# Optimization experiments

Hardware: AMD Instinct MI355X
Metric: run time of the kernel (lower is better)

Reference implementation:

```python
import jax, jax.numpy as jnp
import numpy as np

N_NODES = 100000
N_EDGES = 1600000
IN_FEATS = 128
HEADS = 4
OUT_FEATS = 32
NEG_SLOPE = 0.2


def setup_inputs() -> dict:
    key = jax.random.key(0)
    k1, k2, k3, k4, k5, k6 = jax.random.split(key, 6)
    feat = jax.random.normal(k1, (N_NODES, IN_FEATS), dtype=jnp.float32)
    # nn.Linear(in_feats, out_feats*num_heads).weight -> [H*D_out, D_in]
    W = jax.random.normal(k2, (HEADS * OUT_FEATS, IN_FEATS), dtype=jnp.float32) * (1.0 / np.sqrt(IN_FEATS))
    attn_l = jax.random.normal(k3, (1, HEADS, OUT_FEATS), dtype=jnp.float32) * 0.1
    attn_r = jax.random.normal(k4, (1, HEADS, OUT_FEATS), dtype=jnp.float32) * 0.1
    src = jax.random.randint(k5, (N_EDGES,), 0, N_NODES, dtype=jnp.int32)
    dst = jax.random.randint(k6, (N_EDGES,), 0, N_NODES, dtype=jnp.int32)
    return {"feat": feat, "W": W, "attn_l": attn_l, "attn_r": attn_r, "src": src, "dst": dst}


def reference(feat, W, attn_l, attn_r, src, dst):
    N = feat.shape[0]
    H, D = attn_l.shape[1], attn_l.shape[2]
    # fc: feat @ W.T -> [N, H, D]
    ft = (feat @ W.T).reshape(N, H, D)
    el = jnp.sum(ft * attn_l, axis=-1)  # [N, H]
    er = jnp.sum(ft * attn_r, axis=-1)  # [N, H]
    # SDDMM edge scores (u_add_v) + leaky relu
    e = el[src] + er[dst]  # [E, H]
    e = jnp.where(e > 0, e, NEG_SLOPE * e)
    # segment softmax over edges grouped by destination node
    emax = jax.ops.segment_max(e, dst, num_segments=N)  # [N, H]
    ez = jnp.exp(e - emax[dst])
    esum = jax.ops.segment_sum(ez, dst, num_segments=N)  # [N, H]
    a = ez / esum[dst]  # [E, H]
    # weighted SpMM aggregation (u_mul_e + sum by dst)
    out = jax.ops.segment_sum(ft[src] * a[:, :, None], dst, num_segments=N)  # [N, H, D]
    return out
```

## Files before the change

kernel.cpp:

```cpp
#include <hip/hip_runtime.h>
#include <hip/hip_fp16.h>

#define IN_FEATS 128
#define HEADS 4
#define D_OUT 32
#define HD 128
#define NEG_SLOPE 0.2f

#define BSHIFT 6
#define BSIZE 64
#define CAP 1280
#define NBMAX 1600

#define BSCAT 6
#define MAXCHUNK 3200

typedef _Float16 half8 __attribute__((ext_vector_type(8)));
typedef _Float16 half4v __attribute__((ext_vector_type(4)));
typedef float floatx4 __attribute__((ext_vector_type(4)));

#define LSTR 40
#define OSTR 136
#define SMEM_BYTES (128 * OSTR * 2)

__global__ void init_cursor(int* __restrict__ bcursor, int NB) {
    int b = blockIdx.x * blockDim.x + threadIdx.x;
    if (b < NB) bcursor[b] = b * CAP;
}

__global__ __launch_bounds__(256) void mega(const float* __restrict__ feat,
                                            const float* __restrict__ W,
                                            const float* __restrict__ al,
                                            const float* __restrict__ ar,
                                            const int* __restrict__ src,
                                            const int* __restrict__ dst,
                                            __half* __restrict__ ft_h,
                                            float* __restrict__ el,
                                            float* __restrict__ er,
                                            int* __restrict__ bcursor,
                                            int* __restrict__ bedge,
                                            int N, int E, int NB,
                                            int gemmBlocks, int chunk) {
    __shared__ __align__(16) char smem[SMEM_BYTES];
    const int t = threadIdx.x;

    if (blockIdx.x >= gemmBlocks) {
        int* cnt = (int*)smem;
        int* base = cnt + NBMAX;
        int bid = blockIdx.x - gemmBlocks;
        int e0 = bid * chunk;
        if (e0 >= E) return;
        int e1 = e0 + chunk; if (e1 > E) e1 = E;
        int ne = e1 - e0;
        for (int b = t; b < NB; b += 256) cnt[b] = 0;
        __syncthreads();
        for (int i = t; i < ne; i += 256)
            atomicAdd(&cnt[dst[e0 + i] >> BSHIFT], 1);
        __syncthreads();
        for (int b = t; b < NB; b += 256) {
            int c = cnt[b];
            base[b] = c ? atomicAdd(&bcursor[b], c) : 0;
        }
        __syncthreads();
        for (int b = t; b < NB; b += 256) cnt[b] = 0;
        __syncthreads();
        for (int i = t; i < ne; i += 256) {
            int d = dst[e0 + i];
            int b = d >> BSHIFT;
            int p = base[b] + atomicAdd(&cnt[b], 1);
            if (p < (b + 1) * CAP)
                bedge[p] = src[e0 + i] | ((d & (BSIZE - 1)) << 17);
        }
        return;
    }

    _Float16* sh = (_Float16*)smem;
    _Float16* Als = sh;
    _Float16* Wls = sh + 5120;
    const int w = t >> 6, lane = t & 63, quad = lane >> 4, l15 = lane & 15;
    const int nodeBase = blockIdx.x * 128;

    floatx4 acc[2][8] = {};

    for (int kk = 0; kk < 4; ++kk) {
        const int k0 = kk * 32;
#pragma unroll
        for (int i = 0; i < 4; ++i) {
            int idx = i * 256 + t;
            int row = idx >> 3;
            int q = idx & 7;
            int node = nodeBase + row;
            float4 v = make_float4(0.f, 0.f, 0.f, 0.f);
            if (node < N) v = *(const float4*)(feat + (size_t)node * IN_FEATS + k0 + q * 4);
            half4v hv = {(_Float16)v.x, (_Float16)v.y, (_Float16)v.z, (_Float16)v.w};
            *(half4v*)&Als[row * LSTR + q * 4] = hv;
            float4 wv = *(const float4*)(W + (size_t)row * IN_FEATS + k0 + q * 4);
            half4v hw = {(_Float16)wv.x, (_Float16)wv.y, (_Float16)wv.z, (_Float16)wv.w};
            *(half4v*)&Wls[row * LSTR + q * 4] = hw;
        }
        __syncthreads();
        half8 af0 = *(half8*)&Als[(w * 32 + l15) * LSTR + quad * 8];
        half8 af1 = *(half8*)&Als[(w * 32 + 16 + l15) * LSTR + quad * 8];
        half8 bf[8];
#pragma unroll
        for (int nt = 0; nt < 8; ++nt)
            bf[nt] = *(half8*)&Wls[(nt * 16 + l15) * LSTR + quad * 8];
#pragma unroll
        for (int nt = 0; nt < 8; ++nt) {
            acc[0][nt] = __builtin_amdgcn_mfma_f32_16x16x32_f16(af0, bf[nt], acc[0][nt], 0, 0, 0);
            acc[1][nt] = __builtin_amdgcn_mfma_f32_16x16x32_f16(af1, bf[nt], acc[1][nt], 0, 0, 0);
        }
        __syncthreads();
    }

#pragma unroll
    for (int mt = 0; mt < 2; ++mt)
#pragma unroll
        for (int nt = 0; nt < 8; ++nt)
#pragma unroll
            for (int r = 0; r < 4; ++r)
                sh[(w * 32 + mt * 16 + quad * 4 + r) * OSTR + nt * 16 + l15] =
                    (_Float16)acc[mt][nt][r];
    __syncthreads();

    const int row = t >> 1, seg = t & 1;
    const int node = nodeBase + row;
    half8 hv[8];
#pragma unroll
    for (int j = 0; j < 8; ++j) hv[j] = *(half8*)&sh[row * OSTR + seg * 64 + j * 8];

    float accl0 = 0.f, accl1 = 0.f, accr0 = 0.f, accr1 = 0.f;
#pragma unroll
    for (int j = 0; j < 8; ++j) {
        float4 a0 = *(const float4*)(al + seg * 64 + j * 8);
        float4 a1 = *(const float4*)(al + seg * 64 + j * 8 + 4);
        float4 r0 = *(const float4*)(ar + seg * 64 + j * 8);
        float4 r1 = *(const float4*)(ar + seg * 64 + j * 8 + 4);
        float v0 = (float)hv[j][0], v1 = (float)hv[j][1], v2 = (float)hv[j][2], v3 = (float)hv[j][3];
        float v4 = (float)hv[j][4], v5 = (float)hv[j][5], v6 = (float)hv[j][6], v7 = (float)hv[j][7];
        float dl = v0 * a0.x + v1 * a0.y + v2 * a0.z + v3 * a0.w
                 + v4 * a1.x + v5 * a1.y + v6 * a1.z + v7 * a1.w;
        float dr = v0 * r0.x + v1 * r0.y + v2 * r0.z + v3 * r0.w
                 + v4 * r1.x + v5 * r1.y + v6 * r1.z + v7 * r1.w;
        if (j < 4) { accl0 += dl; accr0 += dr; }
        else       { accl1 += dl; accr1 += dr; }
    }
    if (node < N) {
#pragma unroll
        for (int j = 0; j < 8; ++j)
            *(half8*)(ft_h + (size_t)node * HD + seg * 64 + j * 8) = hv[j];
        el[node * 4 + seg * 2 + 0] = accl0;
        el[node * 4 + seg * 2 + 1] = accl1;
        er[node * 4 + seg * 2 + 0] = accr0;
        er[node * 4 + seg * 2 + 1] = accr1;
    }
}

__global__ __launch_bounds__(256) void bucket_aggregate(const __half* __restrict__ ft_h,
                                                        const float* __restrict__ el,
                                                        const float* __restrict__ er,
                                                        const int* __restrict__ bcursor,
                                                        const int* __restrict__ bedge,
                                                        float* __restrict__ out, int N) {
    __shared__ int eS[CAP];
    __shared__ uint2 eW[CAP];
    __shared__ float4 er4L[BSIZE];
    __shared__ int cnt[BSIZE];
    __shared__ int exs[BSIZE];
    __shared__ int pos[BSIZE];
    const int b = blockIdx.x, t = threadIdx.x;
    const int s0 = b * CAP;
    const int node0 = b << BSHIFT;
    int cntE = bcursor[b] - s0;
    if (cntE > CAP) cntE = CAP;
    if (t < BSIZE) {
        cnt[t] = 0;
        int n = node0 + t;
        er4L[t] = (n < N) ? *(const float4*)(er + (size_t)n * 4)
                          : make_float4(0.f, 0.f, 0.f, 0.f);
    }
    __syncthreads();
    for (int i = t; i < cntE; i += 256)
        atomicAdd(&cnt[bedge[s0 + i] >> 17], 1);
    __syncthreads();
    if (t < BSIZE) {
        int x = cnt[t];
        int inc = x;
#pragma unroll
        for (int off = 1; off < 64; off <<= 1) {
            int y = __shfl_up(inc, off);
            if (t >= off) inc += y;
        }
        exs[t] = inc - x;
        pos[t] = inc - x;
    }
    __syncthreads();
    for (int i = t; i < cntE; i += 256) {
        int v = bedge[s0 + i];
        int dl = v >> 17;
        int s = v & 0x1FFFF;
        float4 el4 = *(const float4*)(el + (size_t)s * 4);
        float4 e4 = er4L[dl];
        float x0 = el4.x + e4.x; x0 = x0 > 0.f ? x0 : NEG_SLOPE * x0;
        float x1 = el4.y + e4.y; x1 = x1 > 0.f ? x1 : NEG_SLOPE * x1;
        float x2 = el4.z + e4.z; x2 = x2 > 0.f ? x2 : NEG_SLOPE * x2;
        float x3 = el4.w + e4.w; x3 = x3 > 0.f ? x3 : NEG_SLOPE * x3;
        __half2 p01 = __floats2half2_rn(__expf(x0), __expf(x1));
        __half2 p23 = __floats2half2_rn(__expf(x2), __expf(x3));
        uint2 pk;
        pk.x = *(unsigned int*)&p01;
        pk.y = *(unsigned int*)&p23;
        int p = atomicAdd(&pos[dl], 1);
        eS[p] = s;
        eW[p] = pk;
    }
    __syncthreads();

    const int wid = t >> 6, lane = t & 63;
    const int g = lane >> 4;
    const int q = lane & 15;
    const int h = q >> 2;
    const unsigned short* eWu = (const unsigned short*)eW;

    for (int dl = wid * 4 + g; dl < BSIZE; dl += 16) {
        int n = node0 + dl;
        const bool alive = n < N;
        int start = alive ? exs[dl] : 0;
        int end = alive ? start + cnt[dl] : 0;

        float a0 = 0.f, a1 = 0.f, a2 = 0.f, a3 = 0.f;
        float a4 = 0.f, a5 = 0.f, a6 = 0.f, a7 = 0.f;
        float ws = 0.f;

        for (int bb = start; bb < end; bb += 8) {
            int4 raw[8];
            float wv[8];
#pragma unroll
            for (int j = 0; j < 8; ++j) {
                int e = bb + j;
                bool v = e < end;
                int s = v ? eS[e] : 0;
                unsigned short u = v ? eWu[e * 4 + h] : (unsigned short)0;
                raw[j] = *(const int4*)(ft_h + (size_t)s * HD + q * 8);
                wv[j] = v ? __half2float(*(__half*)&u) : 0.f;
            }
#pragma unroll
            for (int j = 0; j < 8; ++j) {
                float2 f0 = __half22float2(*(__half2*)&raw[j].x);
                float2 f1 = __half22float2(*(__half2*)&raw[j].y);
                float2 f2 = __half22float2(*(__half2*)&raw[j].z);
                float2 f3 = __half22float2(*(__half2*)&raw[j].w);
                float w0 = wv[j];
                a0 += w0 * f0.x;  a1 += w0 * f0.y;
                a2 += w0 * f1.x;  a3 += w0 * f1.y;
                a4 += w0 * f2.x;  a5 += w0 * f2.y;
                a6 += w0 * f3.x;  a7 += w0 * f3.y;
                ws += w0;
            }
        }
        float inv = ws > 0.f ? 1.0f / ws : 0.f;
        if (alive) {
            float4 o0 = make_float4(a0 * inv, a1 * inv, a2 * inv, a3 * inv);
            float4 o1 = make_float4(a4 * inv, a5 * inv, a6 * inv, a7 * inv);
            float* op = out + (size_t)n * HD + q * 8;
            *(float4*)op = o0;
            *(float4*)(op + 4) = o1;
        }
    }
}

extern "C" void kernel_launch(void* const* d_in, const int* in_sizes, int n_in,
                              void* d_out, int out_size, void* d_ws, size_t ws_size,
                              hipStream_t stream) {
    const float* feat = (const float*)d_in[0];
    const float* W    = (const float*)d_in[1];
    const float* al   = (const float*)d_in[2];
    const float* ar   = (const float*)d_in[3];
    const int* src    = (const int*)d_in[4];
    const int* dst    = (const int*)d_in[5];
    float* out        = (float*)d_out;

    const int N = in_sizes[0] / IN_FEATS;
    const int E = in_sizes[4];
    const int NB = (N + BSIZE - 1) >> BSHIFT;

    char* ws = (char*)d_ws;
    size_t off = 0;
    auto alloc = [&](size_t bytes) {
        void* p = ws + off;
        off += (bytes + 255) & ~(size_t)255;
        return p;
    };
    __half* ft_h   = (__half*)alloc((size_t)N * HD * 2);
    float* el      = (float*)alloc((size_t)N * 4 * 4);
    float* er      = (float*)alloc((size_t)N * 4 * 4);
    int*   bcursor = (int*)alloc((size_t)NBMAX * 4);
    int*   bedge   = (int*)alloc((size_t)NB * CAP * 4);
    (void)ws_size;

    init_cursor<<<(NB + 255) / 256, 256, 0, stream>>>(bcursor, NB);
    int gemmBlocks = (N + 127) / 128;
    int grid2 = 512;
    int chunk = (E + grid2 - 1) / grid2;
    if (chunk > MAXCHUNK) chunk = MAXCHUNK;
    int nblk = (E + chunk - 1) / chunk;
    mega<<<gemmBlocks + nblk, 256, 0, stream>>>(feat, W, al, ar, src, dst,
                                                ft_h, el, er, bcursor, bedge,
                                                N, E, NB, gemmBlocks, chunk);
    bucket_aggregate<<<NB, 256, 0, stream>>>(ft_h, el, er, bcursor, bedge, out, N);
}
```

Measured before the change: 249.4 us.

## Load feat directly into MFMA registers, stage W once swizzled, scatter blocks first

The GEMM part of the fused kernel now converts all of W into shared memory once, using an XOR-swizzled layout, and reads each lane's feat fragments straight from global memory into registers. This removes the per-k-step shared staging of feat and its barriers. The block order is also flipped so the edge-scatter blocks are dispatched before the GEMM blocks, which lets the longer scatter work start early. In exchange, global feat loads become strided per lane (two float4 per row segment), which may coalesce less well than the previous tiled staging.

```diff
diff --git a/kernel.cpp b/kernel.cpp
--- a/kernel.cpp
+++ b/kernel.cpp
@@ -12,14 +12,12 @@
 #define CAP 1280
 #define NBMAX 1600
 
-#define BSCAT 6
 #define MAXCHUNK 3200
 
 typedef _Float16 half8 __attribute__((ext_vector_type(8)));
 typedef _Float16 half4v __attribute__((ext_vector_type(4)));
 typedef float floatx4 __attribute__((ext_vector_type(4)));
 
-#define LSTR 40
 #define OSTR 136
 #define SMEM_BYTES (128 * OSTR * 2)
 
@@ -40,14 +38,14 @@
                                             int* __restrict__ bcursor,
                                             int* __restrict__ bedge,
                                             int N, int E, int NB,
-                                            int gemmBlocks, int chunk) {
+                                            int nblk, int chunk) {
     __shared__ __align__(16) char smem[SMEM_BYTES];
     const int t = threadIdx.x;
 
-    if (blockIdx.x >= gemmBlocks) {
+    if (blockIdx.x < nblk) {
         int* cnt = (int*)smem;
         int* base = cnt + NBMAX;
-        int bid = blockIdx.x - gemmBlocks;
+        int bid = blockIdx.x;
         int e0 = bid * chunk;
         if (e0 >= E) return;
         int e1 = e0 + chunk; if (e1 > E) e1 = E;
@@ -75,43 +73,52 @@
     }
 
     _Float16* sh = (_Float16*)smem;
-    _Float16* Als = sh;
-    _Float16* Wls = sh + 5120;
+    _Float16* Wls = sh;
     const int w = t >> 6, lane = t & 63, quad = lane >> 4, l15 = lane & 15;
-    const int nodeBase = blockIdx.x * 128;
+    const int nodeBase = (blockIdx.x - nblk) * 128;
+
+#pragma unroll
+    for (int i = 0; i < 16; ++i) {
+        int idx = i * 256 + t;
+        int row = idx >> 5;
+        int q = idx & 31;
+        float4 wv = *(const float4*)(W + (size_t)row * IN_FEATS + q * 4);
+        half4v hw = {(_Float16)wv.x, (_Float16)wv.y, (_Float16)wv.z, (_Float16)wv.w};
+        int kb = q >> 1, sub = q & 1;
+        *(half4v*)&Wls[row * 128 + ((kb ^ (row & 7)) << 3) + sub * 4] = hw;
+    }
+    __syncthreads();
 
     floatx4 acc[2][8] = {};
 
+#pragma unroll
     for (int kk = 0; kk < 4; ++kk) {
-        const int k0 = kk * 32;
-#pragma unroll
-        for (int i = 0; i < 4; ++i) {
-            int idx = i * 256 + t;
-            int row = idx >> 3;
-            int q = idx & 7;
-            int node = nodeBase + row;
-            float4 v = make_float4(0.f, 0.f, 0.f, 0.f);
-            if (node < N) v = *(const float4*)(feat + (size_t)node * IN_FEATS + k0 + q * 4);
-            half4v hv = {(_Float16)v.x, (_Float16)v.y, (_Float16)v.z, (_Float16)v.w};
-            *(half4v*)&Als[row * LSTR + q * 4] = hv;
-            float4 wv = *(const float4*)(W + (size_t)row * IN_FEATS + k0 + q * 4);
-            half4v hw = {(_Float16)wv.x, (_Float16)wv.y, (_Float16)wv.z, (_Float16)wv.w};
-            *(half4v*)&Wls[row * LSTR + q * 4] = hw;
-        }
-        __syncthreads();
-        half8 af0 = *(half8*)&Als[(w * 32 + l15) * LSTR + quad * 8];
-        half8 af1 = *(half8*)&Als[(w * 32 + 16 + l15) * LSTR + quad * 8];
+        const int k0 = kk * 32 + quad * 8;
+        half8 a[2];
+#pragma unroll
+        for (int mt = 0; mt < 2; ++mt) {
+            int node = nodeBase + w * 32 + mt * 16 + l15;
+            int nc = node < N ? node : N - 1;
+            const float* fp = feat + (size_t)nc * IN_FEATS + k0;
+            float4 v0 = *(const float4*)fp;
+            float4 v1 = *(const float4*)(fp + 4);
+            a[mt] = half8{(_Float16)v0.x, (_Float16)v0.y, (_Float16)v0.z, (_Float16)v0.w,
+                          (_Float16)v1.x, (_Float16)v1.y, (_Float16)v1.z, (_Float16)v1.w};
+        }
+        const int kb = kk * 4 + quad;
         half8 bf[8];
 #pragma unroll
-        for (int nt = 0; nt < 8; ++nt)
-            bf[nt] = *(half8*)&Wls[(nt * 16 + l15) * LSTR + quad * 8];
-#pragma unroll
         for (int nt = 0; nt < 8; ++nt) {
-            acc[0][nt] = __builtin_amdgcn_mfma_f32_16x16x32_f16(af0, bf[nt], acc[0][nt], 0, 0, 0);
-            acc[1][nt] = __builtin_amdgcn_mfma_f32_16x16x32_f16(af1, bf[nt], acc[1][nt], 0, 0, 0);
-        }
-        __syncthreads();
-    }
+            int rw = nt * 16 + l15;
+            bf[nt] = *(half8*)&Wls[rw * 128 + ((kb ^ (l15 & 7)) << 3)];
+        }
+#pragma unroll
+        for (int nt = 0; nt < 8; ++nt) {
+            acc[0][nt] = __builtin_amdgcn_mfma_f32_16x16x32_f16(a[0], bf[nt], acc[0][nt], 0, 0, 0);
+            acc[1][nt] = __builtin_amdgcn_mfma_f32_16x16x32_f16(a[1], bf[nt], acc[1][nt], 0, 0, 0);
+        }
+    }
+    __syncthreads();
 
 #pragma unroll
     for (int mt = 0; mt < 2; ++mt)
@@ -304,8 +311,8 @@
     int chunk = (E + grid2 - 1) / grid2;
     if (chunk > MAXCHUNK) chunk = MAXCHUNK;
     int nblk = (E + chunk - 1) / chunk;
-    mega<<<gemmBlocks + nblk, 256, 0, stream>>>(feat, W, al, ar, src, dst,
+    mega<<<nblk + gemmBlocks, 256, 0, stream>>>(feat, W, al, ar, src, dst,
                                                 ft_h, el, er, bcursor, bedge,
-                                                N, E, NB, gemmBlocks, chunk);
+                                                N, E, NB, nblk, chunk);
     bucket_aggregate<<<NB, 256, 0, stream>>>(ft_h, el, er, bcursor, bedge, out, N);
 }
```

New measurement: 245.5 us. About the same (-1.6%).
